# Kernel optimization log

Measured on AMD Instinct MI355X. Metric: run time of the kernel, lower is better.

## Reference

```python
import jax, jax.numpy as jnp
import numpy as np

LAMB = 5.0
BETA = 1.0
SWITCH = 1.0
LOG_2PI = float(np.log(2.0 * np.pi))
LOG_PI = float(np.log(np.pi))

N = 524288
H = 100
D = 2
K = 30


def _mlp(x, w1, b1, w2, b2):
    # Linear(2,100) -> ReLU -> Linear(100,2)
    return jax.nn.relu(x @ w1 + b1) @ w2 + b2


def _normal_logprob(x, mu, sigma):
    # torch Normal.log_prob, summed over last dim by Independent(...,1)
    z = (x - mu) / sigma
    return jnp.sum(-0.5 * z * z - jnp.log(sigma) - 0.5 * LOG_2PI, axis=-1)


def _student_t_logprob(x, df, loc, scale):
    # torch StudentT.log_prob, summed over last dim by Independent(...,1)
    y = (x - loc) / scale
    lp = (jax.lax.lgamma(0.5 * (df + 1.0)) - jax.lax.lgamma(0.5 * df)
          - 0.5 * (jnp.log(df) + LOG_PI) - jnp.log(scale)
          - 0.5 * (df + 1.0) * jnp.log1p(y * y / df))
    return jnp.sum(lp, axis=-1)


def setup_inputs() -> dict:
    key = jax.random.key(0)
    ks = jax.random.split(key, 20)
    f32 = jnp.float32

    def lin(k1, k2, din, dout):
        w = jax.random.normal(k1, (din, dout), f32) * (1.0 / np.sqrt(din))
        b = jax.random.normal(k2, (dout,), f32) * 0.01
        return w, b

    inp = {}
    inp["x"] = jax.random.normal(ks[0], (N, D), f32)
    inp["eps"] = jax.random.normal(ks[1], (N, D), f32)
    for i, name in enumerate(["enc_mu", "enc_std", "dec_mu", "dec_df"]):
        w1, b1 = lin(ks[2 + 4 * i], ks[3 + 4 * i], D, H)
        w2, b2 = lin(ks[4 + 4 * i], ks[5 + 4 * i], H, D)
        inp[name + "_w1"], inp[name + "_b1"] = w1, b1
        inp[name + "_w2"], inp[name + "_b2"] = w2, b2
    inp["C"] = jax.random.normal(ks[18], (K, D), f32)
    inp["W"] = jax.random.uniform(ks[19], (K, D), f32)
    return inp


def reference(x, eps,
              enc_mu_w1, enc_mu_b1, enc_mu_w2, enc_mu_b2,
              enc_std_w1, enc_std_b1, enc_std_w2, enc_std_b2,
              dec_mu_w1, dec_mu_b1, dec_mu_w2, dec_mu_b2,
              dec_df_w1, dec_df_b1, dec_df_w2, dec_df_b2,
              C, W):
    z_mu = _mlp(x, enc_mu_w1, enc_mu_b1, enc_mu_w2, enc_mu_b2)
    z_std = jax.nn.softplus(_mlp(x, enc_std_w1, enc_std_b1, enc_std_w2, enc_std_b2))
    sigma = jnp.sqrt(z_std)
    z = z_mu + sigma * eps  # rsample

    x_mu = _mlp(z, dec_mu_w1, dec_mu_b1, dec_mu_w2, dec_mu_b2)
    x_df = jax.nn.softplus(_mlp(z, dec_df_w1, dec_df_b1, dec_df_w2, dec_df_b2))

    # RBF distances z<->C: ||z||^2 + ||C||^2 - 2 z C^T -> [N, K]
    d = (jnp.sum(z * z, axis=1, keepdims=True)
         + jnp.sum(C * C, axis=1) - 2.0 * z @ C.T)
    inv_std = jnp.exp(-LAMB * d) @ jnp.maximum(W, 0.0) + 1e-10  # [N, D]
    x_scale = SWITCH * (1.0 / inv_std) + (1.0 - SWITCH) * 0.02

    log_px = _student_t_logprob(x, x_df, x_mu, x_scale)
    kl = _normal_logprob(z, z_mu, sigma) - _normal_logprob(z, 0.0, 1.0)
    elbo = jnp.mean(log_px - BETA * kl)
    return (elbo, x_mu, x_scale, z, z_mu, z_std)
```

## Files before the change

kernel.cpp:

```cpp
#include <hip/hip_runtime.h>
#include <math.h>

#define LAMB    5.0f
#define LOG_PI  1.144729885849400f
#define L2E     1.4426950408889634f
#define LN2     0.6931471805599453f
#define LAM2E   7.213475204444817f

constexpr int HID = 100;
constexpr int KC  = 30;

typedef float    v2f __attribute__((ext_vector_type(2)));
typedef _Float16 h2  __attribute__((ext_vector_type(2)));

__device__ __forceinline__ v2f splat2(float s) { return (v2f){s, s}; }
__device__ __forceinline__ v2f fma2(v2f a, v2f b, v2f c) { return __builtin_elementwise_fma(a, b, c); }
__device__ __forceinline__ v2f max2(v2f a, v2f b) { return __builtin_elementwise_max(a, b); }

__device__ __forceinline__ float rcp_s(float x)  { return __builtin_amdgcn_rcpf(x); }
__device__ __forceinline__ float lg2_s(float x)  { return __builtin_amdgcn_logf(x); }
__device__ __forceinline__ float ex2_s(float x)  { return __builtin_amdgcn_exp2f(x); }
__device__ __forceinline__ v2f rcp2(v2f x)  { return (v2f){rcp_s(x.x), rcp_s(x.y)}; }
__device__ __forceinline__ v2f exp2v(v2f x) { return (v2f){ex2_s(x.x), ex2_s(x.y)}; }

__device__ __forceinline__ float log1p_s(float u) {
    float big = lg2_s(1.0f + u) * LN2;
    float sml = u * (1.0f - 0.5f * u);
    return (u > 1e-5f) ? big : sml;
}

__device__ __forceinline__ v2f log2_1p2(v2f u) {
    float bx = lg2_s(1.0f + u.x), by = lg2_s(1.0f + u.y);
    float sx = u.x * L2E * (1.0f - 0.5f * u.x);
    float sy = u.y * L2E * (1.0f - 0.5f * u.y);
    return (v2f){ (u.x > 1e-5f) ? bx : sx, (u.y > 1e-5f) ? by : sy };
}

__device__ __forceinline__ float softplus_s(float v) {
    float e = ex2_s(-fabsf(v) * L2E);
    return fmaxf(v, 0.f) + log1p_s(e);
}
__device__ __forceinline__ v2f softplus2(v2f v) {
    return (v2f){softplus_s(v.x), softplus_s(v.y)};
}

__global__ __launch_bounds__(256) void prep(
    const float* __restrict__ Cc,   const float* __restrict__ Wc,
    const float* __restrict__ emw1, const float* __restrict__ emb1,
    const float* __restrict__ emw2,
    const float* __restrict__ esw1, const float* __restrict__ esb1,
    const float* __restrict__ esw2,
    const float* __restrict__ dmw1, const float* __restrict__ dmb1,
    const float* __restrict__ dmw2,
    const float* __restrict__ dfw1, const float* __restrict__ dfb1,
    const float* __restrict__ dfw2,
    float* __restrict__ rbfc, float* __restrict__ encl, h2* __restrict__ hb)
{
    int t = threadIdx.x;
    if (t < KC / 2) {
        int k = 2 * t;
        float c00 = Cc[2 * k],     c01 = Cc[2 * k + 1];
        float c10 = Cc[2 * k + 2], c11 = Cc[2 * k + 3];
        float* p = &rbfc[16 * t];
        p[0] = 2.0f * LAM2E * c00;  p[1] = 2.0f * LAM2E * c10;
        p[2] = 2.0f * LAM2E * c01;  p[3] = 2.0f * LAM2E * c11;
        p[4] = -LAM2E * (c00 * c00 + c01 * c01);
        p[5] = -LAM2E * (c10 * c10 + c11 * c11);
        p[6] = fmaxf(Wc[2 * k],     0.f);  p[7] = fmaxf(Wc[2 * k + 2], 0.f);
        p[8] = fmaxf(Wc[2 * k + 1], 0.f);  p[9] = fmaxf(Wc[2 * k + 3], 0.f);
        p[10] = 0.f; p[11] = 0.f; p[12] = 0.f; p[13] = 0.f; p[14] = 0.f; p[15] = 0.f;
    }
    if (t == 32 || t == 33) {
        const float* w1 = (t == 32) ? emw1 : esw1;
        const float* b1 = (t == 32) ? emb1 : esb1;
        const float* w2 = (t == 32) ? emw2 : esw2;
        float A0 = 0.f, A1 = 0.f, B0 = 0.f, B1 = 0.f, C0 = 0.f, C1 = 0.f;
        for (int j = 0; j < HID; ++j) {
            float w20 = w2[2 * j], w21 = w2[2 * j + 1];
            A0 = fmaf(w1[j],       w20, A0);  A1 = fmaf(w1[j],       w21, A1);
            B0 = fmaf(w1[HID + j], w20, B0);  B1 = fmaf(w1[HID + j], w21, B1);
            C0 = fmaf(b1[j],       w20, C0);  C1 = fmaf(b1[j],       w21, C1);
        }
        float* q = &encl[(t - 32) * 6];
        q[0] = A0; q[1] = A1; q[2] = B0; q[3] = B1; q[4] = C0; q[5] = C1;
    }
    if (t >= 64 && t < 64 + HID / 2) {
        int tt = t - 64;
        int j = 2 * tt;
        h2* p = hb;
        p[tt]       = (h2){(_Float16)dmw1[j],        (_Float16)dmw1[j + 1]};
        p[50 + tt]  = (h2){(_Float16)dmw1[HID + j],  (_Float16)dmw1[HID + j + 1]};
        p[100 + tt] = (h2){(_Float16)dmb1[j],        (_Float16)dmb1[j + 1]};
        p[150 + tt] = (h2){(_Float16)dmw2[2 * j],    (_Float16)dmw2[2 * j + 2]};
        p[200 + tt] = (h2){(_Float16)dmw2[2 * j + 1],(_Float16)dmw2[2 * j + 3]};
    }
    if (t >= 128 && t < 128 + HID / 2) {
        int tt = t - 128;
        int j = 2 * tt;
        h2* p = hb + 256;
        p[tt]       = (h2){(_Float16)dfw1[j],        (_Float16)dfw1[j + 1]};
        p[50 + tt]  = (h2){(_Float16)dfw1[HID + j],  (_Float16)dfw1[HID + j + 1]};
        p[100 + tt] = (h2){(_Float16)dfb1[j],        (_Float16)dfb1[j + 1]};
        p[150 + tt] = (h2){(_Float16)dfw2[2 * j],    (_Float16)dfw2[2 * j + 2]};
        p[200 + tt] = (h2){(_Float16)dfw2[2 * j + 1],(_Float16)dfw2[2 * j + 3]};
    }
}

__global__ __launch_bounds__(256) void vae_main(
    const float* __restrict__ x,    const float* __restrict__ eps,
    const float* __restrict__ emw1, const float* __restrict__ emb1,
    const float* __restrict__ emw2, const float* __restrict__ emb2,
    const float* __restrict__ esw1, const float* __restrict__ esb1,
    const float* __restrict__ esw2, const float* __restrict__ esb2,
    const float* __restrict__ dmb2, const float* __restrict__ dfb2,
    const h2*    __restrict__ hb,
    const float* __restrict__ rbfc, const float* __restrict__ encl,
    float* __restrict__ out_xmu,   float* __restrict__ out_scale,
    float* __restrict__ out_z,     float* __restrict__ out_zmu,
    float* __restrict__ out_zstd,  float* __restrict__ partial,
    int n)
{
    const int i = blockIdx.x * 256 + threadIdx.x;

    float val = 0.0f;

    if (i < n) {
        const v2f xv = *(const v2f*)&x[2 * i];
        const v2f ev = *(const v2f*)&eps[2 * i];
        const v2f vx0 = splat2(xv.x), vx1 = splat2(xv.y);

        v2f accm = splat2(0.f), accs = splat2(0.f);
#pragma unroll 10
        for (int j = 0; j < HID; j += 2) {
            v2f w1a = *(const v2f*)&emw1[j];
            v2f w1b = *(const v2f*)&emw1[HID + j];
            v2f b1  = *(const v2f*)&emb1[j];
            v2f h   = fma2(vx0, w1a, fma2(vx1, w1b, b1));
            v2f w2a = *(const v2f*)&emw2[2 * j];
            v2f w2b = *(const v2f*)&emw2[2 * j + 2];
            accm = fma2(splat2(fabsf(h.x)), w2a, accm);
            accm = fma2(splat2(fabsf(h.y)), w2b, accm);

            v2f s1a = *(const v2f*)&esw1[j];
            v2f s1b = *(const v2f*)&esw1[HID + j];
            v2f sb1 = *(const v2f*)&esb1[j];
            v2f hs  = fma2(vx0, s1a, fma2(vx1, s1b, sb1));
            v2f d0 = *(const v2f*)&esw2[2 * j];
            v2f d1 = *(const v2f*)&esw2[2 * j + 2];
            accs = fma2(splat2(fabsf(hs.x)), d0, accs);
            accs = fma2(splat2(fabsf(hs.y)), d1, accs);
        }
        const v2f linm = fma2(splat2(xv.x), *(const v2f*)&encl[0],
                         fma2(splat2(xv.y), *(const v2f*)&encl[2],
                              *(const v2f*)&encl[4]));
        const v2f lins = fma2(splat2(xv.x), *(const v2f*)&encl[6],
                         fma2(splat2(xv.y), *(const v2f*)&encl[8],
                              *(const v2f*)&encl[10]));
        const v2f zmu  = splat2(0.5f) * (linm + accm) + *(const v2f*)&emb2[0];
        const v2f zstd = softplus2(splat2(0.5f) * (lins + accs) + *(const v2f*)&esb2[0]);
        const v2f sig  = (v2f){__builtin_amdgcn_sqrtf(zstd.x), __builtin_amdgcn_sqrtf(zstd.y)};
        const v2f z    = fma2(sig, ev, zmu);
        const float z0 = z.x, z1 = z.y;

        const _Float16 z0f = (_Float16)z0;
        const _Float16 z1f = (_Float16)z1;
        const h2 z0h = (h2){z0f, z0f};
        const h2 z1h = (h2){z1f, z1f};
        const h2 hzero = {(_Float16)0.f, (_Float16)0.f};
        float dm0 = 0.f, dm1 = 0.f, dg0 = 0.f, dg1 = 0.f;
        const h2* hm = hb;
        const h2* hf = hb + 256;
#pragma unroll 10
        for (int jj = 0; jj < HID / 2; ++jj) {
            h2 pm = __builtin_elementwise_fma(z0h, hm[jj], hm[100 + jj]);
            pm = __builtin_elementwise_fma(z1h, hm[50 + jj], pm);
            pm = __builtin_elementwise_max(pm, hzero);
            dm0 = __builtin_amdgcn_fdot2(pm, hm[150 + jj], dm0, false);
            dm1 = __builtin_amdgcn_fdot2(pm, hm[200 + jj], dm1, false);

            h2 pf = __builtin_elementwise_fma(z0h, hf[jj], hf[100 + jj]);
            pf = __builtin_elementwise_fma(z1h, hf[50 + jj], pf);
            pf = __builtin_elementwise_max(pf, hzero);
            dg0 = __builtin_amdgcn_fdot2(pf, hf[150 + jj], dg0, false);
            dg1 = __builtin_amdgcn_fdot2(pf, hf[200 + jj], dg1, false);
        }
        const v2f xmu = (v2f){dm0, dm1} + *(const v2f*)&dmb2[0];
        const v2f df  = softplus2((v2f){dg0, dg1} + *(const v2f*)&dfb2[0]);

        const float zz = z0 * z0 + z1 * z1;
        const v2f z0s = splat2(z0), z1s = splat2(z1);
        const v2f u0s = splat2(-LAM2E * zz);
        v2f acc0 = splat2(0.f), acc1 = splat2(0.f);
#pragma unroll
        for (int kk = 0; kk < KC / 2; ++kk) {
            const float* p = &rbfc[16 * kk];
            v2f cx = *(const v2f*)&p[0];
            v2f cy = *(const v2f*)&p[2];
            v2f qq = *(const v2f*)&p[4];
            v2f w0p = *(const v2f*)&p[6];
            v2f w1p = *(const v2f*)&p[8];
            v2f arg = fma2(cx, z0s, fma2(cy, z1s, qq + u0s));
            v2f e = exp2v(arg);
            acc0 = fma2(e, w0p, acc0);
            acc1 = fma2(e, w1p, acc1);
        }
        const v2f ia = (v2f){acc0.x + acc0.y, acc1.x + acc1.y} + splat2(1e-10f);
        const v2f vscale = rcp2(ia);

        const v2f a  = splat2(0.5f) * df;
        const v2f b  = a + splat2(3.0f);
        const v2f rb = rcp2(b);
        const v2f t  = splat2(0.5f) * rb;
        const v2f t2 = t * t;
        const v2f p  = t * (splat2(-0.25f) + t2 * (splat2(0.0416666667f) + t2 * splat2(-0.05f)));

        const v2f a1 = a + splat2(1.0f), a2 = a + splat2(2.0f);
        const v2f h1 = a + splat2(0.5f), h2v = a + splat2(1.5f), h3 = a + splat2(2.5f);
        const v2f pn = a * a1 * a2;
        const v2f pd = h1 * h2v * h3;
        const float rprod = (pn.x * pn.y) * rcp_s(pd.x * pd.y);

        const v2f rdf = rcp2(df);
        const float bb_dd = (b.x * b.y) * (rdf.x * rdf.y);
        const float S1 = lg2_s(bb_dd);
        const float S2 = lg2_s(rprod * (ia.x * ia.y));

        const v2f y  = (xv - xmu) * ia;
        const v2f u  = y * y * rdf;
        const v2f L2 = log2_1p2(u);
        const v2f dfp1 = df + splat2(1.0f);

        const float Szstd = lg2_s(zstd.x * zstd.y);

        const float A = 0.5f * S1 + S2
                      - 0.5f * (dfp1.x * L2.x + dfp1.y * L2.y)
                      + 0.5f * Szstd;
        const float ee = ev.x * ev.x + ev.y * ev.y;
        val = LN2 * A + (p.x + p.y) - LOG_PI + 0.5f * ee - 0.5f * zz;

        *(v2f*)&out_xmu[2 * i]   = xmu;
        *(v2f*)&out_scale[2 * i] = vscale;
        *(v2f*)&out_z[2 * i]     = z;
        *(v2f*)&out_zmu[2 * i]   = zmu;
        *(v2f*)&out_zstd[2 * i]  = zstd;
    }

#pragma unroll
    for (int off = 32; off > 0; off >>= 1)
        val += __shfl_down(val, off, 64);

    __shared__ float wsum[4];
    const int lane = threadIdx.x & 63;
    const int wid  = threadIdx.x >> 6;
    if (lane == 0) wsum[wid] = val;
    __syncthreads();
    if (threadIdx.x == 0)
        partial[blockIdx.x] = (wsum[0] + wsum[1]) + (wsum[2] + wsum[3]);
}

__global__ __launch_bounds__(256) void vae_reduce(
    const float* __restrict__ partial, int nblk, float* __restrict__ out, int n)
{
    __shared__ double sh[256];
    double acc = 0.0;
    for (int i = threadIdx.x; i < nblk; i += 256) acc += (double)partial[i];
    sh[threadIdx.x] = acc;
    __syncthreads();
#pragma unroll
    for (int s = 128; s > 0; s >>= 1) {
        if (threadIdx.x < s) sh[threadIdx.x] += sh[threadIdx.x + s];
        __syncthreads();
    }
    if (threadIdx.x == 0) out[0] = (float)(sh[0] / (double)n);
}

extern "C" void kernel_launch(void* const* d_in, const int* in_sizes, int n_in,
                              void* d_out, int out_size, void* d_ws, size_t ws_size,
                              hipStream_t stream) {
    const float* x    = (const float*)d_in[0];
    const float* eps  = (const float*)d_in[1];
    const float* emw1 = (const float*)d_in[2];
    const float* emb1 = (const float*)d_in[3];
    const float* emw2 = (const float*)d_in[4];
    const float* emb2 = (const float*)d_in[5];
    const float* esw1 = (const float*)d_in[6];
    const float* esb1 = (const float*)d_in[7];
    const float* esw2 = (const float*)d_in[8];
    const float* esb2 = (const float*)d_in[9];
    const float* dmw1 = (const float*)d_in[10];
    const float* dmb1 = (const float*)d_in[11];
    const float* dmw2 = (const float*)d_in[12];
    const float* dmb2 = (const float*)d_in[13];
    const float* dfw1 = (const float*)d_in[14];
    const float* dfb1 = (const float*)d_in[15];
    const float* dfw2 = (const float*)d_in[16];
    const float* dfb2 = (const float*)d_in[17];
    const float* Cc   = (const float*)d_in[18];
    const float* Wc   = (const float*)d_in[19];

    const int n = in_sizes[0] / 2;
    float* out = (float*)d_out;
    float* out_elbo  = out;
    float* out_xmu   = out + 1;
    float* out_scale = out + 1 + 2 * (size_t)n;
    float* out_z     = out + 1 + 4 * (size_t)n;
    float* out_zmu   = out + 1 + 6 * (size_t)n;
    float* out_zstd  = out + 1 + 8 * (size_t)n;

    float* partial = (float*)d_ws;
    float* rbfc    = (float*)d_ws + 4096;
    float* encl    = (float*)d_ws + 6144;
    h2*    hb      = (h2*)((float*)d_ws + 8192);

    const int nblk = (n + 255) / 256;

    prep<<<1, 256, 0, stream>>>(Cc, Wc,
                                emw1, emb1, emw2, esw1, esb1, esw2,
                                dmw1, dmb1, dmw2, dfw1, dfb1, dfw2,
                                rbfc, encl, hb);

    vae_main<<<nblk, 256, 0, stream>>>(
        x, eps,
        emw1, emb1, emw2, emb2,
        esw1, esb1, esw2, esb2,
        dmb2, dfb2, hb, rbfc, encl,
        out_xmu, out_scale, out_z, out_zmu, out_zstd,
        partial, n);

    vae_reduce<<<1, 256, 0, stream>>>(partial, nblk, out_elbo, n);
}
```

Before: 43.90 us.

## Split each sample across two lanes and reduce halves with xor shuffles

```diff
diff --git a/kernel.cpp b/kernel.cpp
--- a/kernel.cpp
+++ b/kernel.cpp
@@ -70,6 +70,10 @@
         p[8] = fmaxf(Wc[2 * k + 1], 0.f);  p[9] = fmaxf(Wc[2 * k + 3], 0.f);
         p[10] = 0.f; p[11] = 0.f; p[12] = 0.f; p[13] = 0.f; p[14] = 0.f; p[15] = 0.f;
     }
+    if (t == 15) {
+        float* p = &rbfc[240];
+        for (int q = 0; q < 16; ++q) p[q] = 0.f;
+    }
     if (t == 32 || t == 33) {
         const float* w1 = (t == 32) ? emw1 : esw1;
         const float* b1 = (t == 32) ? emb1 : esb1;
@@ -120,18 +124,22 @@
     float* __restrict__ out_zstd,  float* __restrict__ partial,
     int n)
 {
-    const int i = blockIdx.x * 256 + threadIdx.x;
+    const int tid  = blockIdx.x * 256 + threadIdx.x;
+    const int s    = tid >> 1;
+    const int half = tid & 1;
 
     float val = 0.0f;
 
-    if (i < n) {
-        const v2f xv = *(const v2f*)&x[2 * i];
-        const v2f ev = *(const v2f*)&eps[2 * i];
+    if (s < n) {
+        const v2f xv = *(const v2f*)&x[2 * s];
+        const v2f ev = *(const v2f*)&eps[2 * s];
         const v2f vx0 = splat2(xv.x), vx1 = splat2(xv.y);
 
+        const int o = half * 50;
         v2f accm = splat2(0.f), accs = splat2(0.f);
-#pragma unroll 10
-        for (int j = 0; j < HID; j += 2) {
+#pragma unroll 5
+        for (int jj = 0; jj < 50; jj += 2) {
+            const int j = o + jj;
             v2f w1a = *(const v2f*)&emw1[j];
             v2f w1b = *(const v2f*)&emw1[HID + j];
             v2f b1  = *(const v2f*)&emb1[j];
@@ -150,6 +158,11 @@
             accs = fma2(splat2(fabsf(hs.x)), d0, accs);
             accs = fma2(splat2(fabsf(hs.y)), d1, accs);
         }
+        accm.x += __shfl_xor(accm.x, 1, 64);
+        accm.y += __shfl_xor(accm.y, 1, 64);
+        accs.x += __shfl_xor(accs.x, 1, 64);
+        accs.y += __shfl_xor(accs.y, 1, 64);
+
         const v2f linm = fma2(splat2(xv.x), *(const v2f*)&encl[0],
                          fma2(splat2(xv.y), *(const v2f*)&encl[2],
                               *(const v2f*)&encl[4]));
@@ -168,10 +181,10 @@
         const h2 z1h = (h2){z1f, z1f};
         const h2 hzero = {(_Float16)0.f, (_Float16)0.f};
         float dm0 = 0.f, dm1 = 0.f, dg0 = 0.f, dg1 = 0.f;
-        const h2* hm = hb;
-        const h2* hf = hb + 256;
-#pragma unroll 10
-        for (int jj = 0; jj < HID / 2; ++jj) {
+        const h2* hm = hb + half * 25;
+        const h2* hf = hb + 256 + half * 25;
+#pragma unroll 5
+        for (int jj = 0; jj < 25; ++jj) {
             h2 pm = __builtin_elementwise_fma(z0h, hm[jj], hm[100 + jj]);
             pm = __builtin_elementwise_fma(z1h, hm[50 + jj], pm);
             pm = __builtin_elementwise_max(pm, hzero);
@@ -184,6 +197,10 @@
             dg0 = __builtin_amdgcn_fdot2(pf, hf[150 + jj], dg0, false);
             dg1 = __builtin_amdgcn_fdot2(pf, hf[200 + jj], dg1, false);
         }
+        dm0 += __shfl_xor(dm0, 1, 64);
+        dm1 += __shfl_xor(dm1, 1, 64);
+        dg0 += __shfl_xor(dg0, 1, 64);
+        dg1 += __shfl_xor(dg1, 1, 64);
         const v2f xmu = (v2f){dm0, dm1} + *(const v2f*)&dmb2[0];
         const v2f df  = softplus2((v2f){dg0, dg1} + *(const v2f*)&dfb2[0]);
 
@@ -191,9 +208,10 @@
         const v2f z0s = splat2(z0), z1s = splat2(z1);
         const v2f u0s = splat2(-LAM2E * zz);
         v2f acc0 = splat2(0.f), acc1 = splat2(0.f);
+        const float* rb_base = rbfc + half * 128;
 #pragma unroll
-        for (int kk = 0; kk < KC / 2; ++kk) {
-            const float* p = &rbfc[16 * kk];
+        for (int kk = 0; kk < 8; ++kk) {
+            const float* p = &rb_base[16 * kk];
             v2f cx = *(const v2f*)&p[0];
             v2f cy = *(const v2f*)&p[2];
             v2f qq = *(const v2f*)&p[4];
@@ -204,7 +222,11 @@
             acc0 = fma2(e, w0p, acc0);
             acc1 = fma2(e, w1p, acc1);
         }
-        const v2f ia = (v2f){acc0.x + acc0.y, acc1.x + acc1.y} + splat2(1e-10f);
+        float ia0 = acc0.x + acc0.y;
+        float ia1 = acc1.x + acc1.y;
+        ia0 += __shfl_xor(ia0, 1, 64);
+        ia1 += __shfl_xor(ia1, 1, 64);
+        const v2f ia = (v2f){ia0, ia1} + splat2(1e-10f);
         const v2f vscale = rcp2(ia);
 
         const v2f a  = splat2(0.5f) * df;
@@ -236,34 +258,31 @@
                       - 0.5f * (dfp1.x * L2.x + dfp1.y * L2.y)
                       + 0.5f * Szstd;
         const float ee = ev.x * ev.x + ev.y * ev.y;
-        val = LN2 * A + (p.x + p.y) - LOG_PI + 0.5f * ee - 0.5f * zz;
-
-        *(v2f*)&out_xmu[2 * i]   = xmu;
-        *(v2f*)&out_scale[2 * i] = vscale;
-        *(v2f*)&out_z[2 * i]     = z;
-        *(v2f*)&out_zmu[2 * i]   = zmu;
-        *(v2f*)&out_zstd[2 * i]  = zstd;
+        val = 0.5f * (LN2 * A + (p.x + p.y) - LOG_PI + 0.5f * ee - 0.5f * zz);
+
+        if (half == 0) {
+            *(v2f*)&out_xmu[2 * s]   = xmu;
+            *(v2f*)&out_scale[2 * s] = vscale;
+            *(v2f*)&out_z[2 * s]     = z;
+        } else {
+            *(v2f*)&out_zmu[2 * s]   = zmu;
+            *(v2f*)&out_zstd[2 * s]  = zstd;
+        }
     }
 
 #pragma unroll
     for (int off = 32; off > 0; off >>= 1)
         val += __shfl_down(val, off, 64);
-
-    __shared__ float wsum[4];
-    const int lane = threadIdx.x & 63;
-    const int wid  = threadIdx.x >> 6;
-    if (lane == 0) wsum[wid] = val;
-    __syncthreads();
-    if (threadIdx.x == 0)
-        partial[blockIdx.x] = (wsum[0] + wsum[1]) + (wsum[2] + wsum[3]);
+    if ((threadIdx.x & 63) == 0)
+        partial[blockIdx.x * 4 + (threadIdx.x >> 6)] = val;
 }
 
 __global__ __launch_bounds__(256) void vae_reduce(
-    const float* __restrict__ partial, int nblk, float* __restrict__ out, int n)
+    const float* __restrict__ partial, int nprt, float* __restrict__ out, int n)
 {
     __shared__ double sh[256];
     double acc = 0.0;
-    for (int i = threadIdx.x; i < nblk; i += 256) acc += (double)partial[i];
+    for (int i = threadIdx.x; i < nprt; i += 256) acc += (double)partial[i];
     sh[threadIdx.x] = acc;
     __syncthreads();
 #pragma unroll
@@ -307,19 +326,20 @@
     float* out_zmu   = out + 1 + 6 * (size_t)n;
     float* out_zstd  = out + 1 + 8 * (size_t)n;
 
+    const int nblk2 = (2 * n + 255) / 256;
+    const int nprt  = nblk2 * 4;
+
     float* partial = (float*)d_ws;
-    float* rbfc    = (float*)d_ws + 4096;
-    float* encl    = (float*)d_ws + 6144;
-    h2*    hb      = (h2*)((float*)d_ws + 8192);
-
-    const int nblk = (n + 255) / 256;
+    float* rbfc    = (float*)d_ws + 16384;
+    float* encl    = (float*)d_ws + 16704;
+    h2*    hb      = (h2*)((float*)d_ws + 17024);
 
     prep<<<1, 256, 0, stream>>>(Cc, Wc,
                                 emw1, emb1, emw2, esw1, esb1, esw2,
                                 dmw1, dmb1, dmw2, dfw1, dfb1, dfw2,
                                 rbfc, encl, hb);
 
-    vae_main<<<nblk, 256, 0, stream>>>(
+    vae_main<<<nblk2, 256, 0, stream>>>(
         x, eps,
         emw1, emb1, emw2, emb2,
         esw1, esb1, esw2, esb2,
@@ -327,5 +347,5 @@
         out_xmu, out_scale, out_z, out_zmu, out_zstd,
         partial, n);
 
-    vae_reduce<<<1, 256, 0, stream>>>(partial, nblk, out_elbo, n);
-}
+    vae_reduce<<<1, 256, 0, stream>>>(partial, nprt, out_elbo, n);
+}
```

New measurement: 164.8 us. +275.5%, slower.

## Fuse final ELBO reduction into main kernel via packed fixed-point atomic counter

Applied to the files above, without the earlier changes.

```diff
diff --git a/kernel.cpp b/kernel.cpp
--- a/kernel.cpp
+++ b/kernel.cpp
@@ -54,9 +54,11 @@
     const float* __restrict__ dmw2,
     const float* __restrict__ dfw1, const float* __restrict__ dfb1,
     const float* __restrict__ dfw2,
-    float* __restrict__ rbfc, float* __restrict__ encl, h2* __restrict__ hb)
+    float* __restrict__ rbfc, float* __restrict__ encl, h2* __restrict__ hb,
+    unsigned long long* __restrict__ acc_ctr)
 {
     int t = threadIdx.x;
+    if (t == 255) *acc_ctr = 0ull;
     if (t < KC / 2) {
         int k = 2 * t;
         float c00 = Cc[2 * k],     c01 = Cc[2 * k + 1];
@@ -115,9 +117,10 @@
     const float* __restrict__ dmb2, const float* __restrict__ dfb2,
     const h2*    __restrict__ hb,
     const float* __restrict__ rbfc, const float* __restrict__ encl,
-    float* __restrict__ out_xmu,   float* __restrict__ out_scale,
-    float* __restrict__ out_z,     float* __restrict__ out_zmu,
-    float* __restrict__ out_zstd,  float* __restrict__ partial,
+    float* __restrict__ out_elbo,  float* __restrict__ out_xmu,
+    float* __restrict__ out_scale, float* __restrict__ out_z,
+    float* __restrict__ out_zmu,   float* __restrict__ out_zstd,
+    unsigned long long* __restrict__ acc_ctr,
     int n)
 {
     const int i = blockIdx.x * 256 + threadIdx.x;
@@ -254,24 +257,21 @@
     const int wid  = threadIdx.x >> 6;
     if (lane == 0) wsum[wid] = val;
     __syncthreads();
-    if (threadIdx.x == 0)
-        partial[blockIdx.x] = (wsum[0] + wsum[1]) + (wsum[2] + wsum[3]);
-}
-
-__global__ __launch_bounds__(256) void vae_reduce(
-    const float* __restrict__ partial, int nblk, float* __restrict__ out, int n)
-{
-    __shared__ double sh[256];
-    double acc = 0.0;
-    for (int i = threadIdx.x; i < nblk; i += 256) acc += (double)partial[i];
-    sh[threadIdx.x] = acc;
-    __syncthreads();
-#pragma unroll
-    for (int s = 128; s > 0; s >>= 1) {
-        if (threadIdx.x < s) sh[threadIdx.x] += sh[threadIdx.x + s];
-        __syncthreads();
-    }
-    if (threadIdx.x == 0) out[0] = (float)(sh[0] / (double)n);
+
+    if (threadIdx.x == 0) {
+        float ps = (wsum[0] + wsum[1]) + (wsum[2] + wsum[3]);
+        double fx = ((double)ps + 131072.0) * 131072.0;
+        long long fixed = (long long)fx;
+        if (fixed < 0) fixed = 0;
+        if (fixed > ((1ll << 47) - 1)) fixed = (1ll << 47) - 1;
+        unsigned long long add = (1ull << 52) | (unsigned long long)fixed;
+        unsigned long long old = atomicAdd(acc_ctr, add);
+        if ((old >> 52) == (unsigned long long)(gridDim.x - 1)) {
+            unsigned long long tot = (old & ((1ull << 52) - 1)) + (unsigned long long)fixed;
+            double sum = (double)tot / 131072.0 - (double)gridDim.x * 131072.0;
+            out_elbo[0] = (float)(sum / (double)n);
+        }
+    }
 }
 
 extern "C" void kernel_launch(void* const* d_in, const int* in_sizes, int n_in,
@@ -307,7 +307,7 @@
     float* out_zmu   = out + 1 + 6 * (size_t)n;
     float* out_zstd  = out + 1 + 8 * (size_t)n;
 
-    float* partial = (float*)d_ws;
+    unsigned long long* acc_ctr = (unsigned long long*)d_ws;
     float* rbfc    = (float*)d_ws + 4096;
     float* encl    = (float*)d_ws + 6144;
     h2*    hb      = (h2*)((float*)d_ws + 8192);
@@ -317,15 +317,13 @@
     prep<<<1, 256, 0, stream>>>(Cc, Wc,
                                 emw1, emb1, emw2, esw1, esb1, esw2,
                                 dmw1, dmb1, dmw2, dfw1, dfb1, dfw2,
-                                rbfc, encl, hb);
+                                rbfc, encl, hb, acc_ctr);
 
     vae_main<<<nblk, 256, 0, stream>>>(
         x, eps,
         emw1, emb1, emw2, emb2,
         esw1, esb1, esw2, esb2,
         dmb2, dfb2, hb, rbfc, encl,
-        out_xmu, out_scale, out_z, out_zmu, out_zstd,
-        partial, n);
-
-    vae_reduce<<<1, 256, 0, stream>>>(partial, nblk, out_elbo, n);
-}
+        out_elbo, out_xmu, out_scale, out_z, out_zmu, out_zstd,
+        acc_ctr, n);
+}
```

Measured after the change: 55.34 us. +26.1%, slower.
